# Kernel optimization log

Hardware: AMD Instinct MI355X
Metric: run time of the kernel (lower is better)

The kernel has to match this reference:

```python
import jax, jax.numpy as jnp
import numpy as np

L, N, E, D_MODEL, H = 3, 50000, 600000, 128, 8
D = D_MODEL // H          # per-head dim = 16
DFF = 4 * D_MODEL         # feedforward hidden = 512


def prelu(x, a):
    return jnp.where(x >= 0, x, a * x)


def layernorm(x, scale, bias, eps=1e-5):
    m = x.mean(-1, keepdims=True)
    v = x.var(-1, keepdims=True)
    return (x - m) * jax.lax.rsqrt(v + eps) * scale + bias


def setup_inputs() -> dict:
    key = jax.random.key(0)
    ks = jax.random.split(key, 16)
    s = 1.0 / np.sqrt(D_MODEL)
    return {
        "in_feats": jax.random.normal(ks[0], (N, D_MODEL), jnp.float32),
        "src": jax.random.randint(ks[1], (E,), 0, N, jnp.int32),
        "dst": jax.random.randint(ks[2], (E,), 0, N, jnp.int32),
        # per-layer stacked parameters
        "W": jax.random.normal(ks[3], (L, D_MODEL, D_MODEL), jnp.float32) * s,
        "attn_l": jax.random.normal(ks[4], (L, H, D), jnp.float32) * s,
        "attn_r": jax.random.normal(ks[5], (L, H, D), jnp.float32) * s,
        "conv_bias": jnp.zeros((L, H, D), jnp.float32),
        "a_conv": jnp.full((L,), 0.25, jnp.float32),   # PReLU slope after conv
        "ln_scale": jnp.ones((L, D_MODEL), jnp.float32),
        "ln_bias": jnp.zeros((L, D_MODEL), jnp.float32),
        "W1": jax.random.normal(ks[6], (L, D_MODEL, DFF), jnp.float32) * s,
        "b1": jnp.zeros((L, DFF), jnp.float32),
        "W2": jax.random.normal(ks[7], (L, DFF, D_MODEL), jnp.float32) / np.sqrt(DFF),
        "b2": jnp.zeros((L, D_MODEL), jnp.float32),
        "a_ff": jnp.full((L,), 0.25, jnp.float32),     # PReLU slope in FF
    }


def _gat_conv(x, src, dst, W, attn_l, attn_r, conv_bias, a_conv):
    # DGL GATConv: project, per-edge additive attention, edge-softmax over dst, scatter.
    z = (x @ W).reshape(N, H, D)                    # [N,H,D]
    el = (z * attn_l).sum(-1)                       # [N,H]
    er = (z * attn_r).sum(-1)                       # [N,H]
    e = jax.nn.leaky_relu(el[src] + er[dst], 0.2)   # [E,H]
    emax = jax.ops.segment_max(e, dst, num_segments=N)
    emax = jnp.where(jnp.isfinite(emax), emax, 0.0)  # zero in-degree guard
    ex = jnp.exp(e - emax[dst])                     # [E,H]
    denom = jax.ops.segment_sum(ex, dst, num_segments=N)  # [N,H]
    msg = ex[:, :, None] * z[src]                   # [E,H,D]
    agg = jax.ops.segment_sum(msg, dst, num_segments=N)   # [N,H,D]
    out = agg / jnp.maximum(denom, 1e-9)[:, :, None]
    out = prelu(out + conv_bias, a_conv)            # bias + PReLU activation
    return out.reshape(N, H * D)


def reference(in_feats, src, dst, W, attn_l, attn_r, conv_bias, a_conv,
              ln_scale, ln_bias, W1, b1, W2, b2, a_ff):
    outputs = []
    x = in_feats
    for l in range(L):
        h = _gat_conv(x, src, dst, W[l], attn_l[l], attn_r[l], conv_bias[l], a_conv[l])
        h = layernorm(h, ln_scale[l], ln_bias[l])   # layer['norm']
        # FeedForward, norm_first=True, sharing the same LayerNorm params
        hn = layernorm(h, ln_scale[l], ln_bias[l])
        ff = prelu(hn @ W1[l] + b1[l], a_ff[l]) @ W2[l] + b2[l]
        x = h + ff
        outputs.append(x)
    return jnp.stack(outputs)                       # [L, N, d]
```

## Files before the change

### kernel.cpp

```cpp
#include <hip/hip_runtime.h>

#define DM 128
#define NH 8
#define DFF 512

typedef __attribute__((ext_vector_type(8))) short bf16x8;
typedef __attribute__((ext_vector_type(4))) float f32x4;
typedef __attribute__((ext_vector_type(2))) unsigned uintx2;

#define WAITVM(N) do { asm volatile("s_waitcnt vmcnt(" #N ")" ::: "memory"); \
                       __builtin_amdgcn_sched_barrier(0); } while (0)
#define WAITLGKM0 do { asm volatile("s_waitcnt lgkmcnt(0)" ::: "memory"); \
                       __builtin_amdgcn_sched_barrier(0); } while (0)

__device__ __forceinline__ short f2bf(float f) {
    union { float f; unsigned u; } v; v.f = f;
    unsigned r = v.u + 0x7fffu + ((v.u >> 16) & 1u);
    return (short)(r >> 16);
}
__device__ __forceinline__ float bf2f(unsigned short b) {
    union { unsigned u; float f; } v; v.u = ((unsigned)b) << 16; return v.f;
}

template<int ROWS, int NT>
__device__ __forceinline__ void stage_tile(
    const short* __restrict__ g, int row0, int maxrow, int rstride, int kbase,
    short* s, int tid)
{
    const int lane = tid & 63;
#pragma unroll
    for (int rr = 0; rr < ROWS * 16 / NT; ++rr) {
        int idx = rr * NT + tid;
        int row = idx >> 4, kc = idx & 15;
        int rg = row0 + row;
        rg = (rg < maxrow) ? rg : (maxrow - 1);
        const short* src = g + (size_t)rg * rstride + kbase
                         + ((kc ^ (row & 15)) << 3);
        short* dst = s + (size_t)(idx - lane) * 8;
        __builtin_amdgcn_global_load_lds(
            (const __attribute__((address_space(1))) void*)src,
            (__attribute__((address_space(3))) void*)dst, 16, 0, 0);
    }
}

__device__ __forceinline__ bf16x8 frag_ld(const short* s, int row, int ks, int g)
{
    return *(const bf16x8*)(s + row * 128 + ((((ks << 2) + g) ^ (row & 15)) << 3));
}

__device__ __forceinline__ bf16x8 frag_ld_h(const short* s, int row, int c,
                                            int ks, int g)
{
    int ch = ((ks << 2) + g) ^ (row & 15);
    return *(const bf16x8*)(s + row * 512 + c * 128 + (ch << 3));
}

template<bool PRELU, int NOUT>
__global__ __launch_bounds__(512, 4) void gemm_k128_stream(
    const short* __restrict__ A, const short* __restrict__ Bt,
    const float* __restrict__ bias, const float* __restrict__ affp,
    int M, short* __restrict__ outbf)
{
    __shared__ __align__(16) short sW[128 * 128];
    __shared__ __align__(16) short sA[3][64 * 128];

    const int tid = threadIdx.x;
    const int wave = tid >> 6, lane = tid & 63;
    const int wm = wave >> 2, wn = wave & 3;
    const int bn = blockIdx.x * 128;
    const int fr = lane & 15, g = lane >> 4;
    const int lr4 = g << 2;
    const int nT = (M + 63) >> 6;
    const int GY = gridDim.y;
    const int t0 = blockIdx.y;
    const int nLoc = (t0 < nT) ? ((nT - 1 - t0) / GY + 1) : 0;

    float bb[2]; float aff = 0.0f;
    if constexpr (PRELU) {
        aff = *affp;
#pragma unroll
        for (int cg = 0; cg < 2; ++cg)
            bb[cg] = bias[bn + wn * 32 + cg * 16 + fr];
    }

    stage_tile<128, 512>(Bt + (size_t)bn * 128, 0, 128, 128, 0, sW, tid);
    if (nLoc > 0) stage_tile<64, 512>(A, t0 * 64, M, 128, 0, sA[0], tid);
    if (nLoc > 1) stage_tile<64, 512>(A, (t0 + GY) * 64, M, 128, 0, sA[1], tid);

    for (int i = 0; i < nLoc; ++i) {
        const int t = t0 + i * GY;
        if (i >= 1 && i + 1 < nLoc)
            stage_tile<64, 512>(A, (t + GY) * 64, M, 128, 0, sA[(i + 1) % 3], tid);

        if (i == 0) { if (nLoc > 1) { WAITVM(2); } else { WAITVM(0); } }
        else if (i + 1 < nLoc) { WAITVM(18); }
        else { WAITVM(16); }
        __builtin_amdgcn_s_barrier();

        const short* sAb = sA[i % 3];
        f32x4 acc[2][2];
#pragma unroll
        for (int ii = 0; ii < 2; ++ii)
#pragma unroll
            for (int cg = 0; cg < 2; ++cg) acc[ii][cg] = (f32x4)0.0f;

#pragma unroll
        for (int ks = 0; ks < 4; ++ks) {
            bf16x8 af[2], bf[2];
#pragma unroll
            for (int ii = 0; ii < 2; ++ii)
                af[ii] = frag_ld(sAb, wm * 32 + ii * 16 + fr, ks, g);
#pragma unroll
            for (int cg = 0; cg < 2; ++cg)
                bf[cg] = frag_ld(sW, wn * 32 + cg * 16 + fr, ks, g);
#pragma unroll
            for (int ii = 0; ii < 2; ++ii)
#pragma unroll
                for (int cg = 0; cg < 2; ++cg)
                    acc[ii][cg] = __builtin_amdgcn_mfma_f32_16x16x32_bf16(
                        af[ii], bf[cg], acc[ii][cg], 0, 0, 0);
        }

#pragma unroll
        for (int ii = 0; ii < 2; ++ii)
#pragma unroll
            for (int cg = 0; cg < 2; ++cg) {
                int colL = wn * 32 + cg * 16 + fr;
#pragma unroll
                for (int r = 0; r < 4; ++r) {
                    int row = t * 64 + wm * 32 + ii * 16 + lr4 + r;
                    if (row < M) {
                        float v = acc[ii][cg][r];
                        if constexpr (PRELU) {
                            v += bb[cg];
                            v = (v >= 0.0f) ? v : aff * v;
                        }
                        outbf[(size_t)row * NOUT + bn + colL] = f2bf(v);
                    }
                }
            }
    }
}

__global__ __launch_bounds__(512, 2) void ffn12z(
    const short* __restrict__ hn, const short* __restrict__ W1t,
    const short* __restrict__ W2t, const short* __restrict__ h_bf,
    const float* __restrict__ b1, const float* __restrict__ b2,
    const float* __restrict__ affp, const short* __restrict__ Wnt,
    int has_next, int M, float* __restrict__ xo, short* __restrict__ z_next)
{
    __shared__ __align__(16) short sH[64 * 512];
    __shared__ __align__(16) short sW[2][128 * 128];

    const int tid = threadIdx.x;
    const int wave = tid >> 6, lane = tid & 63;
    const int wm = wave >> 2, wn = wave & 3;
    const int bm = blockIdx.x * 64;
    const int fr = lane & 15, g = lane >> 4;
    const int lr4 = g << 2, fk8 = g << 3;

    stage_tile<128, 512>(W1t, 0, 512, 128, 0, sW[0], tid);

    bf16x8 ah[2][4];
#pragma unroll
    for (int ii = 0; ii < 2; ++ii) {
        int row = bm + wm * 32 + ii * 16 + fr;
        row = (row < M) ? row : (M - 1);
#pragma unroll
        for (int ks = 0; ks < 4; ++ks)
            ah[ii][ks] = *(const bf16x8*)(hn + (size_t)row * DM + ks * 32 + fk8);
    }
    float aff = *affp;

    f32x4 acc2[2][2];
#pragma unroll
    for (int ii = 0; ii < 2; ++ii)
#pragma unroll
        for (int cg = 0; cg < 2; ++cg) acc2[ii][cg] = (f32x4)0.0f;

#pragma unroll
    for (int j = 0; j < 9; ++j) {
        if (j >= 1) { WAITLGKM0; __builtin_amdgcn_s_barrier(); }
        if (j + 1 < 9) {
            int jj = j + 1;
            if (jj < 4)
                stage_tile<128, 512>(W1t, jj * 128, 512, 128, 0, sW[jj & 1], tid);
            else if (jj < 8)
                stage_tile<128, 512>(W2t, 0, 128, 512, (jj - 4) * 128, sW[jj & 1], tid);
            else
                stage_tile<128, 512>(Wnt, 0, 128, 128, 0, sW[jj & 1], tid);
            WAITVM(4);
        } else {
            WAITVM(0);
        }
        __builtin_amdgcn_s_barrier();

        if (j < 4) {
            f32x4 a1[2][2];
#pragma unroll
            for (int ii = 0; ii < 2; ++ii)
#pragma unroll
                for (int cg = 0; cg < 2; ++cg) a1[ii][cg] = (f32x4)0.0f;
#pragma unroll
            for (int ks = 0; ks < 4; ++ks) {
                bf16x8 bf[2];
#pragma unroll
                for (int cg = 0; cg < 2; ++cg)
                    bf[cg] = frag_ld(sW[j & 1], wn * 32 + cg * 16 + fr, ks, g);
#pragma unroll
                for (int ii = 0; ii < 2; ++ii)
#pragma unroll
                    for (int cg = 0; cg < 2; ++cg)
                        a1[ii][cg] = __builtin_amdgcn_mfma_f32_16x16x32_bf16(
                            ah[ii][ks], bf[cg], a1[ii][cg], 0, 0, 0);
            }
#pragma unroll
            for (int ii = 0; ii < 2; ++ii)
#pragma unroll
                for (int cg = 0; cg < 2; ++cg) {
                    int colC = wn * 32 + cg * 16 + fr;
                    float bb = b1[j * 128 + colC];
#pragma unroll
                    for (int r = 0; r < 4; ++r) {
                        int rowL = wm * 32 + ii * 16 + lr4 + r;
                        float v = a1[ii][cg][r] + bb;
                        v = (v >= 0.0f) ? v : aff * v;
                        int ch = (colC >> 3) ^ (rowL & 15);
                        sH[rowL * 512 + j * 128 + (ch << 3) + (colC & 7)] = f2bf(v);
                    }
                }
        } else if (j < 8) {
            int c = j - 4;
#pragma unroll
            for (int ks = 0; ks < 4; ++ks) {
                bf16x8 af[2], bf[2];
#pragma unroll
                for (int ii = 0; ii < 2; ++ii)
                    af[ii] = frag_ld_h(sH, wm * 32 + ii * 16 + fr, c, ks, g);
#pragma unroll
                for (int cg = 0; cg < 2; ++cg)
                    bf[cg] = frag_ld(sW[j & 1], wn * 32 + cg * 16 + fr, ks, g);
#pragma unroll
                for (int ii = 0; ii < 2; ++ii)
#pragma unroll
                    for (int cg = 0; cg < 2; ++cg)
                        acc2[ii][cg] = __builtin_amdgcn_mfma_f32_16x16x32_bf16(
                            af[ii], bf[cg], acc2[ii][cg], 0, 0, 0);
            }
        } else {
#pragma unroll
            for (int ii = 0; ii < 2; ++ii)
#pragma unroll
                for (int cg = 0; cg < 2; ++cg) {
                    int colL = wn * 32 + cg * 16 + fr;
                    float bbv = b2[colL];
#pragma unroll
                    for (int r = 0; r < 4; ++r) {
                        int rowL = wm * 32 + ii * 16 + lr4 + r;
                        int row = bm + rowL;
                        int rc = (row < M) ? row : (M - 1);
                        float v = acc2[ii][cg][r] + bbv
                                + bf2f((unsigned short)h_bf[(size_t)rc * DM + colL]);
                        if (row < M) xo[(size_t)row * DM + colL] = v;
                        if (has_next) {
                            int kc = colL >> 3;
                            sH[rowL * 128 + ((kc ^ (rowL & 15)) << 3) + (colL & 7)]
                                = f2bf(v);
                        }
                    }
                }
            if (has_next) {
                WAITLGKM0;
                __builtin_amdgcn_s_barrier();
                f32x4 a3[2][2];
#pragma unroll
                for (int ii = 0; ii < 2; ++ii)
#pragma unroll
                    for (int cg = 0; cg < 2; ++cg) a3[ii][cg] = (f32x4)0.0f;
#pragma unroll
                for (int ks = 0; ks < 4; ++ks) {
                    bf16x8 af[2], bf[2];
#pragma unroll
                    for (int ii = 0; ii < 2; ++ii)
                        af[ii] = frag_ld(sH, wm * 32 + ii * 16 + fr, ks, g);
#pragma unroll
                    for (int cg = 0; cg < 2; ++cg)
                        bf[cg] = frag_ld(sW[0], wn * 32 + cg * 16 + fr, ks, g);
#pragma unroll
                    for (int ii = 0; ii < 2; ++ii)
#pragma unroll
                        for (int cg = 0; cg < 2; ++cg)
                            a3[ii][cg] = __builtin_amdgcn_mfma_f32_16x16x32_bf16(
                                af[ii], bf[cg], a3[ii][cg], 0, 0, 0);
                }
#pragma unroll
                for (int ii = 0; ii < 2; ++ii)
#pragma unroll
                    for (int cg = 0; cg < 2; ++cg) {
                        int colL = wn * 32 + cg * 16 + fr;
#pragma unroll
                        for (int r = 0; r < 4; ++r) {
                            int row = bm + wm * 32 + ii * 16 + lr4 + r;
                            if (row < M)
                                z_next[(size_t)row * DM + colL] = f2bf(a3[ii][cg][r]);
                        }
                    }
            }
        }
    }
}

__global__ void conv_all_kernel(
    const float* __restrict__ W, const float* __restrict__ W1,
    const float* __restrict__ W2, const float* __restrict__ xin,
    short* __restrict__ Wt, short* __restrict__ W1t, short* __restrict__ W2t,
    short* __restrict__ xbf, int nFeat, int nL)
{
    int idx = blockIdx.x * blockDim.x + threadIdx.x;
    const int n0 = nL * DM * DM, n1 = nL * DM * DFF, n2 = nL * DFF * DM;
    if (idx < n0) {
        int l = idx / (DM * DM), rem = idx & (DM * DM - 1);
        int r = rem >> 7, c = rem & 127;
        Wt[(size_t)l * DM * DM + c * DM + r] = f2bf(W[idx]);
        return;
    }
    idx -= n0;
    if (idx < n1) {
        int l = idx / (DM * DFF), rem = idx & (DM * DFF - 1);
        int r = rem >> 9, c = rem & 511;
        W1t[(size_t)l * DM * DFF + (size_t)c * DM + r] = f2bf(W1[idx]);
        return;
    }
    idx -= n1;
    if (idx < n2) {
        int l = idx / (DFF * DM), rem = idx & (DFF * DM - 1);
        int r = rem >> 7, c = rem & 127;
        W2t[(size_t)l * DFF * DM + (size_t)c * DFF + r] = f2bf(W2[idx]);
        return;
    }
    idx -= n2;
    if (idx < nFeat) xbf[idx] = f2bf(xin[idx]);
}

__global__ void el_er_kernel(const short* __restrict__ z,
                             const float* __restrict__ al,
                             const float* __restrict__ ar,
                             float* __restrict__ el, float* __restrict__ er, int N)
{
    int idx = blockIdx.x * blockDim.x + threadIdx.x;
    if (idx >= N * NH) return;
    int n = idx >> 3, h = idx & 7;
    const unsigned* zp = (const unsigned*)(z + (size_t)n * DM + h * 16);
    const float* alp = al + h * 16;
    const float* arp = ar + h * 16;
    float sl = 0.0f, sr = 0.0f;
#pragma unroll
    for (int d2 = 0; d2 < 8; ++d2) {
        unsigned u = zp[d2];
        float z0 = bf2f((unsigned short)(u & 0xffff));
        float z1 = bf2f((unsigned short)(u >> 16));
        sl = fmaf(z0, alp[2 * d2], sl);     sl = fmaf(z1, alp[2 * d2 + 1], sl);
        sr = fmaf(z0, arp[2 * d2], sr);     sr = fmaf(z1, arp[2 * d2 + 1], sr);
    }
    el[idx] = sl;
    er[idx] = sr;
}

__global__ void hist_kernel(const int* __restrict__ dst, int* __restrict__ deg, int E)
{
    int e = blockIdx.x * blockDim.x + threadIdx.x;
    if (e < E) atomicAdd(&deg[dst[e]], 1);
}

__global__ void scan1_kernel(const int* __restrict__ deg, int* __restrict__ incl,
                             int* __restrict__ bsum, int N)
{
    __shared__ int sm[256];
    int i = blockIdx.x * 256 + threadIdx.x;
    int v = (i < N) ? deg[i] : 0;
    sm[threadIdx.x] = v;
    __syncthreads();
    for (int off = 1; off < 256; off <<= 1) {
        int t = (threadIdx.x >= off) ? sm[threadIdx.x - off] : 0;
        __syncthreads();
        sm[threadIdx.x] += t;
        __syncthreads();
    }
    if (i < N) incl[i] = sm[threadIdx.x];
    if (threadIdx.x == 255) bsum[blockIdx.x] = sm[255];
}

__global__ void scan2_kernel(int* __restrict__ bsum, int nb)
{
    __shared__ int sm[256];
    int v = (threadIdx.x < nb) ? bsum[threadIdx.x] : 0;
    sm[threadIdx.x] = v;
    __syncthreads();
    for (int off = 1; off < 256; off <<= 1) {
        int t = (threadIdx.x >= off) ? sm[threadIdx.x - off] : 0;
        __syncthreads();
        sm[threadIdx.x] += t;
        __syncthreads();
    }
    if (threadIdx.x < nb) bsum[threadIdx.x] = sm[threadIdx.x];
}

__global__ void scan3_kernel(const int* __restrict__ incl, const int* __restrict__ bsum,
                             int* __restrict__ row_ptr, int N)
{
    int i = blockIdx.x * 256 + threadIdx.x;
    if (i < N) {
        int off = (blockIdx.x > 0) ? bsum[blockIdx.x - 1] : 0;
        row_ptr[i + 1] = incl[i] + off;
    }
    if (i == 0) row_ptr[0] = 0;
}

__global__ void scatter_kernel(const int* __restrict__ src, const int* __restrict__ dst,
                               const int* __restrict__ row_ptr, int* __restrict__ cursor,
                               int* __restrict__ csr_src, int E)
{
    int e = blockIdx.x * blockDim.x + threadIdx.x;
    if (e >= E) return;
    int t = dst[e];
    int pos = atomicAdd(&cursor[t], 1);
    csr_src[row_ptr[t] + pos] = src[e];
}

__global__ __launch_bounds__(256) void gat_agg_ln_kernel(
    const int* __restrict__ row_ptr, const int* __restrict__ csr_src,
    const short* __restrict__ z, const float* __restrict__ el,
    const float* __restrict__ er, const float* __restrict__ cb,
    const float* __restrict__ a_conv,
    const float* __restrict__ scale, const float* __restrict__ bias,
    short* __restrict__ h_out, short* __restrict__ hn_out, int N)
{
    int wave = threadIdx.x >> 6, lane = threadIdx.x & 63;
    int half = lane >> 5, l32 = lane & 31;
    int t = blockIdx.x * 8 + wave * 2 + half;
    if (t >= N) return;
    int h = l32 >> 2;
    int cbase = l32 * 4;
    float er_t = er[t * NH + h];
    int e0 = row_ptr[t], e1 = row_ptr[t + 1];
    float a0 = 0.0f, a1 = 0.0f, a2 = 0.0f, a3 = 0.0f, den = 0.0f;

    int e = e0;
    int s[8];
    bool have = (e + 8 <= e1);
    if (have) {
#pragma unroll
        for (int k = 0; k < 8; ++k) s[k] = csr_src[e + k];
    }
    while (have) {
        float x[8]; uintx2 u[8];
#pragma unroll
        for (int k = 0; k < 8; ++k) x[k] = el[s[k] * NH + h];
#pragma unroll
        for (int k = 0; k < 8; ++k)
            u[k] = *(const uintx2*)(z + (size_t)s[k] * DM + cbase);
        int en = e + 8;
        bool hv2 = (en + 8 <= e1);
        int sn[8];
#pragma unroll
        for (int k = 0; k < 8; ++k) sn[k] = hv2 ? csr_src[en + k] : 0;
#pragma unroll
        for (int k = 0; k < 8; ++k) {
            float v = x[k] + er_t;
            v = (v >= 0.0f) ? v : 0.2f * v;
            float w = __expf(v);
            den += w;
            unsigned w0 = u[k][0], w1 = u[k][1];
            a0 = fmaf(w, bf2f((unsigned short)(w0 & 0xffff)), a0);
            a1 = fmaf(w, bf2f((unsigned short)(w0 >> 16)),    a1);
            a2 = fmaf(w, bf2f((unsigned short)(w1 & 0xffff)), a2);
            a3 = fmaf(w, bf2f((unsigned short)(w1 >> 16)),    a3);
        }
#pragma unroll
        for (int k = 0; k < 8; ++k) s[k] = sn[k];
        e = en; have = hv2;
    }
    for (; e + 4 <= e1; e += 4) {
        int s4[4];
#pragma unroll
        for (int k = 0; k < 4; ++k) s4[k] = csr_src[e + k];
        float x[4]; uintx2 u[4];
#pragma unroll
        for (int k = 0; k < 4; ++k) x[k] = el[s4[k] * NH + h];
#pragma unroll
        for (int k = 0; k < 4; ++k)
            u[k] = *(const uintx2*)(z + (size_t)s4[k] * DM + cbase);
#pragma unroll
        for (int k = 0; k < 4; ++k) {
            float v = x[k] + er_t;
            v = (v >= 0.0f) ? v : 0.2f * v;
            float w = __expf(v);
            den += w;
            unsigned w0 = u[k][0], w1 = u[k][1];
            a0 = fmaf(w, bf2f((unsigned short)(w0 & 0xffff)), a0);
            a1 = fmaf(w, bf2f((unsigned short)(w0 >> 16)),    a1);
            a2 = fmaf(w, bf2f((unsigned short)(w1 & 0xffff)), a2);
            a3 = fmaf(w, bf2f((unsigned short)(w1 >> 16)),    a3);
        }
    }
    for (; e < e1; ++e) {
        int sv = csr_src[e];
        float v = el[sv * NH + h] + er_t;
        v = (v >= 0.0f) ? v : 0.2f * v;
        float w = __expf(v);
        den += w;
        uintx2 u = *(const uintx2*)(z + (size_t)sv * DM + cbase);
        unsigned w0 = u[0], w1 = u[1];
        a0 = fmaf(w, bf2f((unsigned short)(w0 & 0xffff)), a0);
        a1 = fmaf(w, bf2f((unsigned short)(w0 >> 16)),    a1);
        a2 = fmaf(w, bf2f((unsigned short)(w1 & 0xffff)), a2);
        a3 = fmaf(w, bf2f((unsigned short)(w1 >> 16)),    a3);
    }

    float a = *a_conv;
    float inv = 1.0f / fmaxf(den, 1e-9f);
    float o[4] = { a0 * inv + cb[cbase],     a1 * inv + cb[cbase + 1],
                   a2 * inv + cb[cbase + 2], a3 * inv + cb[cbase + 3] };
#pragma unroll
    for (int j = 0; j < 4; ++j) o[j] = (o[j] >= 0.0f) ? o[j] : a * o[j];

    float sc[4], bi[4];
#pragma unroll
    for (int j = 0; j < 4; ++j) { sc[j] = scale[cbase + j]; bi[j] = bias[cbase + j]; }

    float s1 = o[0] + o[1] + o[2] + o[3];
    float ss = o[0]*o[0] + o[1]*o[1] + o[2]*o[2] + o[3]*o[3];
#pragma unroll
    for (int off = 16; off > 0; off >>= 1) {
        s1 += __shfl_xor(s1, off, 64);
        ss += __shfl_xor(ss, off, 64);
    }
    float mean = s1 * (1.0f / 128.0f);
    float var = ss * (1.0f / 128.0f) - mean * mean;
    float rstd = rsqrtf(var + 1e-5f);
    float hv[4];
#pragma unroll
    for (int j = 0; j < 4; ++j) hv[j] = (o[j] - mean) * rstd * sc[j] + bi[j];
    {
        uintx2 p;
        p[0] = (unsigned)(unsigned short)f2bf(hv[0])
             | ((unsigned)(unsigned short)f2bf(hv[1]) << 16);
        p[1] = (unsigned)(unsigned short)f2bf(hv[2])
             | ((unsigned)(unsigned short)f2bf(hv[3]) << 16);
        *(uintx2*)(h_out + (size_t)t * DM + cbase) = p;
    }

    s1 = hv[0] + hv[1] + hv[2] + hv[3];
    ss = hv[0]*hv[0] + hv[1]*hv[1] + hv[2]*hv[2] + hv[3]*hv[3];
#pragma unroll
    for (int off = 16; off > 0; off >>= 1) {
        s1 += __shfl_xor(s1, off, 64);
        ss += __shfl_xor(ss, off, 64);
    }
    mean = s1 * (1.0f / 128.0f);
    var = ss * (1.0f / 128.0f) - mean * mean;
    rstd = rsqrtf(var + 1e-5f);
    {
        uintx2 p;
        float n0 = (hv[0] - mean) * rstd * sc[0] + bi[0];
        float n1 = (hv[1] - mean) * rstd * sc[1] + bi[1];
        float n2 = (hv[2] - mean) * rstd * sc[2] + bi[2];
        float n3 = (hv[3] - mean) * rstd * sc[3] + bi[3];
        p[0] = (unsigned)(unsigned short)f2bf(n0)
             | ((unsigned)(unsigned short)f2bf(n1) << 16);
        p[1] = (unsigned)(unsigned short)f2bf(n2)
             | ((unsigned)(unsigned short)f2bf(n3) << 16);
        *(uintx2*)(hn_out + (size_t)t * DM + cbase) = p;
    }
}

extern "C" void kernel_launch(void* const* d_in, const int* in_sizes, int n_in,
                              void* d_out, int out_size, void* d_ws, size_t ws_size,
                              hipStream_t stream)
{
    const float* in_feats = (const float*)d_in[0];
    const int*   src      = (const int*)d_in[1];
    const int*   dst      = (const int*)d_in[2];
    const float* W        = (const float*)d_in[3];
    const float* attn_l   = (const float*)d_in[4];
    const float* attn_r   = (const float*)d_in[5];
    const float* convb    = (const float*)d_in[6];
    const float* a_conv   = (const float*)d_in[7];
    const float* ln_scale = (const float*)d_in[8];
    const float* ln_bias  = (const float*)d_in[9];
    const float* W1       = (const float*)d_in[10];
    const float* b1       = (const float*)d_in[11];
    const float* W2       = (const float*)d_in[12];
    const float* b2       = (const float*)d_in[13];
    const float* a_ff     = (const float*)d_in[14];
    float* out = (float*)d_out;

    const int N = in_sizes[0] / DM;
    const int E = in_sizes[1];
    const int L = in_sizes[7];

    char* wsb = (char*)d_ws;
    size_t off = 0;
    auto alloc = [&](size_t bytes) { char* p = wsb + off; off += (bytes + 255) & ~(size_t)255; return p; };

    short* z_bf  = (short*)alloc((size_t)N * DM * sizeof(short));
    short* h_bf  = (short*)alloc((size_t)N * DM * sizeof(short));
    short* hn_bf = (short*)alloc((size_t)N * DM * sizeof(short));
    short* x_bf  = (short*)alloc((size_t)N * DM * sizeof(short));
    float* el    = (float*)alloc((size_t)N * NH * sizeof(float));
    float* er    = (float*)alloc((size_t)N * NH * sizeof(float));
    short* Wt    = (short*)alloc((size_t)L * DM * DM * sizeof(short));
    short* W1t   = (short*)alloc((size_t)L * DFF * DM * sizeof(short));
    short* W2t   = (short*)alloc((size_t)L * DM * DFF * sizeof(short));
    int* deg     = (int*)alloc((size_t)N * sizeof(int));
    int* incl    = (int*)alloc((size_t)N * sizeof(int));
    int* bsum    = (int*)alloc(256 * sizeof(int));
    int* row_ptr = (int*)alloc((size_t)(N + 1) * sizeof(int));
    int* cursor  = (int*)alloc((size_t)N * sizeof(int));
    int* csr_src = (int*)alloc((size_t)E * sizeof(int));

    const int gM64  = (N + 63) / 64;
    const int nbScan = (N + 255) / 256;

    hipMemsetAsync(deg, 0, (size_t)N * sizeof(int), stream);
    hipMemsetAsync(cursor, 0, (size_t)N * sizeof(int), stream);
    hist_kernel<<<(E + 255) / 256, 256, 0, stream>>>(dst, deg, E);
    scan1_kernel<<<nbScan, 256, 0, stream>>>(deg, incl, bsum, N);
    scan2_kernel<<<1, 256, 0, stream>>>(bsum, nbScan);
    scan3_kernel<<<nbScan, 256, 0, stream>>>(incl, bsum, row_ptr, N);
    scatter_kernel<<<(E + 255) / 256, 256, 0, stream>>>(src, dst, row_ptr, cursor, csr_src, E);

    {
        int total = L * DM * DM + L * DM * DFF + L * DFF * DM + N * DM;
        conv_all_kernel<<<(total + 255) / 256, 256, 0, stream>>>(
            W, W1, W2, in_feats, Wt, W1t, W2t, x_bf, N * DM, L);
    }

    gemm_k128_stream<false, DM><<<dim3(1, 512), 512, 0, stream>>>(
        x_bf, Wt, nullptr, nullptr, N, z_bf);
    el_er_kernel<<<(N * NH + 255) / 256, 256, 0, stream>>>(
        z_bf, attn_l, attn_r, el, er, N);

    for (int l = 0; l < L; ++l) {
        float* xo = out + (size_t)l * N * DM;
        const int has_next = (l + 1 < L) ? 1 : 0;
        const short* Wnt = has_next ? (Wt + (size_t)(l + 1) * DM * DM) : Wt;

        gat_agg_ln_kernel<<<(N + 7) / 8, 256, 0, stream>>>(
            row_ptr, csr_src, z_bf, el, er, convb + (size_t)l * DM, a_conv + l,
            ln_scale + (size_t)l * DM, ln_bias + (size_t)l * DM, h_bf, hn_bf, N);

        ffn12z<<<gM64, 512, 0, stream>>>(
            hn_bf, W1t + (size_t)l * DFF * DM, W2t + (size_t)l * DM * DFF,
            h_bf, b1 + (size_t)l * DFF, b2 + (size_t)l * DM, a_ff + l,
            Wnt, has_next, N, xo, z_bf);

        if (has_next)
            el_er_kernel<<<(N * NH + 255) / 256, 256, 0, stream>>>(
                z_bf, attn_l + (size_t)(l + 1) * NH * 16,
                attn_r + (size_t)(l + 1) * NH * 16, el, er, N);
    }
}
```

Baseline: 498.2 us.

## Interleave FFN W1/W2 chunks to shrink hidden-activation LDS and raise occupancy

The fused FFN kernel now alternates W1 and W2 chunk stages, so each 128-wide slice of the hidden activation is produced and consumed right away. This shrinks the hidden buffer in LDS from 64x512 to 64x128 and raises the launch-bounds occupancy target from 2 to 4 blocks per CU. Bias and residual values are prefetched into registers before the weight pipeline starts. The trade-off is more barriers per chunk and extra register pressure at the higher occupancy target, which could cause spills.

```diff
diff --git a/kernel.cpp b/kernel.cpp
--- a/kernel.cpp
+++ b/kernel.cpp
@@ -46,13 +46,6 @@
 __device__ __forceinline__ bf16x8 frag_ld(const short* s, int row, int ks, int g)
 {
     return *(const bf16x8*)(s + row * 128 + ((((ks << 2) + g) ^ (row & 15)) << 3));
-}
-
-__device__ __forceinline__ bf16x8 frag_ld_h(const short* s, int row, int c,
-                                            int ks, int g)
-{
-    int ch = ((ks << 2) + g) ^ (row & 15);
-    return *(const bf16x8*)(s + row * 512 + c * 128 + (ch << 3));
 }
 
 template<bool PRELU, int NOUT>
@@ -142,15 +135,15 @@
     }
 }
 
-__global__ __launch_bounds__(512, 2) void ffn12z(
+__global__ __launch_bounds__(512, 4) void ffn12z(
     const short* __restrict__ hn, const short* __restrict__ W1t,
     const short* __restrict__ W2t, const short* __restrict__ h_bf,
     const float* __restrict__ b1, const float* __restrict__ b2,
     const float* __restrict__ affp, const short* __restrict__ Wnt,
     int has_next, int M, float* __restrict__ xo, short* __restrict__ z_next)
 {
-    __shared__ __align__(16) short sH[64 * 512];
     __shared__ __align__(16) short sW[2][128 * 128];
+    __shared__ __align__(16) short sH[64 * 128];
 
     const int tid = threadIdx.x;
     const int wave = tid >> 6, lane = tid & 63;
@@ -159,8 +152,6 @@
     const int fr = lane & 15, g = lane >> 4;
     const int lr4 = g << 2, fk8 = g << 3;
 
-    stage_tile<128, 512>(W1t, 0, 512, 128, 0, sW[0], tid);
-
     bf16x8 ah[2][4];
 #pragma unroll
     for (int ii = 0; ii < 2; ++ii) {
@@ -170,8 +161,31 @@
         for (int ks = 0; ks < 4; ++ks)
             ah[ii][ks] = *(const bf16x8*)(hn + (size_t)row * DM + ks * 32 + fk8);
     }
+    unsigned short hres[2][2][4];
+    float bb2[2];
+#pragma unroll
+    for (int ii = 0; ii < 2; ++ii)
+#pragma unroll
+        for (int cg = 0; cg < 2; ++cg) {
+            int colL = wn * 32 + cg * 16 + fr;
+            if (ii == 0) bb2[cg] = b2[colL];
+#pragma unroll
+            for (int r = 0; r < 4; ++r) {
+                int row = bm + wm * 32 + ii * 16 + lr4 + r;
+                int rc = (row < M) ? row : (M - 1);
+                hres[ii][cg][r] = *(const unsigned short*)(h_bf + (size_t)rc * DM + colL);
+            }
+        }
+    float bb1[4][2];
+#pragma unroll
+    for (int c = 0; c < 4; ++c)
+#pragma unroll
+        for (int cg = 0; cg < 2; ++cg)
+            bb1[c][cg] = b1[c * 128 + wn * 32 + cg * 16 + fr];
     float aff = *affp;
 
+    stage_tile<128, 512>(W1t, 0, 512, 128, 0, sW[0], tid);
+
     f32x4 acc2[2][2];
 #pragma unroll
     for (int ii = 0; ii < 2; ++ii)
@@ -179,23 +193,27 @@
         for (int cg = 0; cg < 2; ++cg) acc2[ii][cg] = (f32x4)0.0f;
 
 #pragma unroll
-    for (int j = 0; j < 9; ++j) {
-        if (j >= 1) { WAITLGKM0; __builtin_amdgcn_s_barrier(); }
-        if (j + 1 < 9) {
-            int jj = j + 1;
-            if (jj < 4)
-                stage_tile<128, 512>(W1t, jj * 128, 512, 128, 0, sW[jj & 1], tid);
-            else if (jj < 8)
-                stage_tile<128, 512>(W2t, 0, 128, 512, (jj - 4) * 128, sW[jj & 1], tid);
-            else
-                stage_tile<128, 512>(Wnt, 0, 128, 128, 0, sW[jj & 1], tid);
+    for (int q = 0; q < 9; ++q) {
+        __builtin_amdgcn_s_barrier();
+        if (q < 8) {
+            const int jj = q + 1;
+            if (jj < 8) {
+                const int c = jj >> 1;
+                if ((jj & 1) == 0)
+                    stage_tile<128, 512>(W1t, c * 128, 512, 128, 0, sW[jj & 1], tid);
+                else
+                    stage_tile<128, 512>(W2t, 0, 128, DFF, c * 128, sW[jj & 1], tid);
+            } else {
+                stage_tile<128, 512>(Wnt, 0, 128, DM, 0, sW[0], tid);
+            }
             WAITVM(4);
         } else {
             WAITVM(0);
         }
         __builtin_amdgcn_s_barrier();
 
-        if (j < 4) {
+        if (q < 8 && (q & 1) == 0) {
+            const int c = q >> 1;
             f32x4 a1[2][2];
 #pragma unroll
             for (int ii = 0; ii < 2; ++ii)
@@ -206,7 +224,7 @@
                 bf16x8 bf[2];
 #pragma unroll
                 for (int cg = 0; cg < 2; ++cg)
-                    bf[cg] = frag_ld(sW[j & 1], wn * 32 + cg * 16 + fr, ks, g);
+                    bf[cg] = frag_ld(sW[0], wn * 32 + cg * 16 + fr, ks, g);
 #pragma unroll
                 for (int ii = 0; ii < 2; ++ii)
 #pragma unroll
@@ -219,27 +237,25 @@
 #pragma unroll
                 for (int cg = 0; cg < 2; ++cg) {
                     int colC = wn * 32 + cg * 16 + fr;
-                    float bb = b1[j * 128 + colC];
 #pragma unroll
                     for (int r = 0; r < 4; ++r) {
                         int rowL = wm * 32 + ii * 16 + lr4 + r;
-                        float v = a1[ii][cg][r] + bb;
+                        float v = a1[ii][cg][r] + bb1[c][cg];
                         v = (v >= 0.0f) ? v : aff * v;
                         int ch = (colC >> 3) ^ (rowL & 15);
-                        sH[rowL * 512 + j * 128 + (ch << 3) + (colC & 7)] = f2bf(v);
+                        sH[rowL * 128 + (ch << 3) + (colC & 7)] = f2bf(v);
                     }
                 }
-        } else if (j < 8) {
-            int c = j - 4;
+        } else if (q < 8) {
 #pragma unroll
             for (int ks = 0; ks < 4; ++ks) {
                 bf16x8 af[2], bf[2];
 #pragma unroll
                 for (int ii = 0; ii < 2; ++ii)
-                    af[ii] = frag_ld_h(sH, wm * 32 + ii * 16 + fr, c, ks, g);
+                    af[ii] = frag_ld(sH, wm * 32 + ii * 16 + fr, ks, g);
 #pragma unroll
                 for (int cg = 0; cg < 2; ++cg)
-                    bf[cg] = frag_ld(sW[j & 1], wn * 32 + cg * 16 + fr, ks, g);
+                    bf[cg] = frag_ld(sW[1], wn * 32 + cg * 16 + fr, ks, g);
 #pragma unroll
                 for (int ii = 0; ii < 2; ++ii)
 #pragma unroll
@@ -253,14 +269,11 @@
 #pragma unroll
                 for (int cg = 0; cg < 2; ++cg) {
                     int colL = wn * 32 + cg * 16 + fr;
-                    float bbv = b2[colL];
 #pragma unroll
                     for (int r = 0; r < 4; ++r) {
                         int rowL = wm * 32 + ii * 16 + lr4 + r;
                         int row = bm + rowL;
-                        int rc = (row < M) ? row : (M - 1);
-                        float v = acc2[ii][cg][r] + bbv
-                                + bf2f((unsigned short)h_bf[(size_t)rc * DM + colL]);
+                        float v = acc2[ii][cg][r] + bb2[cg] + bf2f(hres[ii][cg][r]);
                         if (row < M) xo[(size_t)row * DM + colL] = v;
                         if (has_next) {
                             int kc = colL >> 3;
@@ -307,6 +320,7 @@
                     }
             }
         }
+        WAITLGKM0;
     }
 }
 
```

After: 552.7 us. 1.11x slower.
